# Performance work log

Hardware: AMD Instinct MI355X
Metric: run time of the kernel (lower is better)

Reference implementation:

```python
import jax, jax.numpy as jnp
import numpy as np

B = 32        # number of graphs
NPG = 2048    # nodes per graph (equal sizes -> max_size == NPG)
N = B * NPG   # total nodes
DEG = 16      # average degree
E = N * DEG   # total edges
F_IN = 128    # num_node_feats
LATENT = [32, 32, 32, 1]
TOTAL = sum(LATENT)  # 97
K = 30        # phi output size (DGCNN k)
OUT = 32      # output_dim


def setup_inputs() -> dict:
    key = jax.random.key(0)
    ks = jax.random.split(key, 16)
    node_feat = jax.random.normal(ks[0], (N, F_IN), jnp.float32)

    # edges constrained within each graph (block-diagonal n2n adjacency)
    rng = np.random.default_rng(0)
    offsets = np.repeat(np.arange(B, dtype=np.int64) * NPG, NPG * DEG)
    src = rng.integers(0, NPG, size=E) + offsets
    dst = rng.integers(0, NPG, size=E) + offsets
    edge_index = jnp.asarray(np.stack([src, dst]).astype(np.int32))

    # node_degs = in-degree + 1, shape [N, 1]
    degs = np.bincount(dst, minlength=N).astype(np.float32)
    node_degs = jnp.asarray(degs + 1.0)[:, None]

    def lin(k, fan_in, fan_out):
        s = 1.0 / np.sqrt(fan_in)
        kw, kb = jax.random.split(k)
        W = jax.random.uniform(kw, (fan_in, fan_out), jnp.float32, -s, s)
        b = jax.random.uniform(kb, (fan_out,), jnp.float32, -s, s)
        return W, b

    dims = [F_IN] + LATENT
    params = {}
    for i in range(len(LATENT)):
        W, b = lin(ks[1 + i], dims[i], dims[i + 1])
        params[f"W{i}"] = W
        params[f"b{i}"] = b
    params["phi_W"], params["phi_b"] = lin(ks[10], TOTAL, K)
    params["rho_W"], params["rho_b"] = lin(ks[11], K, OUT)

    return dict(node_feat=node_feat, node_degs=node_degs, edge_index=edge_index, **params)


def reference(node_feat, node_degs, W0, b0, W1, b1, W2, b2, W3, b3,
              phi_W, phi_b, rho_W, rho_b, edge_index):
    src, dst = edge_index[0], edge_index[1]
    n = node_feat.shape[0]

    def spmm(x):  # n2n adjacency @ x via gather + segment-sum
        return jax.ops.segment_sum(x[src], dst, num_segments=n)

    h = node_feat
    layers = [(W0, b0), (W1, b1), (W2, b2), (W3, b3)]
    cats = []
    for W, b in layers:
        pooled = spmm(h) + h                       # A h + h
        h = jnp.tanh((pooled @ W + b) / node_degs)  # linear, degree norm, tanh
        cats.append(h)
    msg = jnp.concatenate(cats, axis=1)            # [N, 97]

    # sortpooling-to-batched tensor: equal graph sizes -> pure reshape
    batched = msg.reshape(B, NPG, TOTAL)

    # DeepSets invariant model: rho(sum_i phi(x_i))
    phi = jax.nn.relu(batched @ phi_W + phi_b)     # [B, NPG, K]
    summed = jnp.sum(phi, axis=1)                  # [B, K]
    out = summed @ rho_W + rho_b                   # [B, OUT]
    return out
```

## Files before the change

### kernel.cpp

```cpp
#include <hip/hip_runtime.h>
#include <hip/hip_bf16.h>

#define NN 65536
#define NE (NN * 16)
#define NG 32
#define MAXD 64

#define WS_CURSOR 0
#define WS_SUMMED 262144
#define WS_ELL    1048576
#define WS_ZA     (WS_ELL + NN * MAXD * 4)
#define WS_ZB     (WS_ZA + NN * 32 * 2)
#define WS_H1     (WS_ZB + NN * 32 * 2)
#define WS_H2     (WS_H1 + NN * 32 * 2)
#define WS_H3     (WS_H2 + NN * 32 * 2)
#define WS_Z4     (WS_H3 + NN * 32 * 2)

typedef unsigned short bf16;

__device__ __forceinline__ int xcd_swz(int b, int chunk) {
    return (b & 7) * chunk + (b >> 3);
}

__device__ __forceinline__ float ftanh(float x) {
    float xc = fmaxf(fminf(x, 15.f), -15.f);
    float e = __expf(2.f * xc);
    return (e - 1.f) * __builtin_amdgcn_rcpf(e + 1.f);
}

__device__ __forceinline__ float bf2f(bf16 u) {
    return __uint_as_float(((unsigned int)u) << 16);
}
__device__ __forceinline__ bf16 f2bf(float x) {
    unsigned int b = __float_as_uint(x);
    b += 0x7FFF + ((b >> 16) & 1);
    return (bf16)(b >> 16);
}

__global__ __launch_bounds__(256) void k_build(const int* __restrict__ ei,
                                               int* __restrict__ cursor,
                                               int* __restrict__ ell) {
    int blk = xcd_swz(blockIdx.x, 128);
    int idx = blk * 256 + threadIdx.x;
    const int4* e4 = (const int4*)ei;
    int4 s = e4[idx];
    int4 d = e4[NE / 4 + idx];
    int t;
    t = atomicAdd(&cursor[d.x], 1); if (t < MAXD) ell[d.x * MAXD + t] = s.x;
    t = atomicAdd(&cursor[d.y], 1); if (t < MAXD) ell[d.y * MAXD + t] = s.y;
    t = atomicAdd(&cursor[d.z], 1); if (t < MAXD) ell[d.z * MAXD + t] = s.z;
    t = atomicAdd(&cursor[d.w], 1); if (t < MAXD) ell[d.w * MAXD + t] = s.w;
}

__global__ __launch_bounds__(256) void k_gemm1(const float* __restrict__ feat,
                                               const float* __restrict__ W0,
                                               bf16* __restrict__ z1) {
    __shared__ float wl[32 * 132];
    __shared__ float hl[64 * 132];
    int tid = threadIdx.x;
    for (int i = tid; i < 128 * 32; i += 256) {
        int k = i >> 5, c = i & 31;
        wl[c * 132 + k] = W0[i];
    }
    int base = blockIdx.x * 64;
    const float* fsrc = feat + (size_t)base * 128;
    #pragma unroll
    for (int v = 0; v < 8; ++v) {
        int flat = v * 1024 + tid * 4;
        int rr = flat >> 7, kk = flat & 127;
        *(float4*)&hl[rr * 132 + kk] = *(const float4*)&fsrc[flat];
    }
    __syncthreads();
    int cg = tid & 15, rg = tid >> 4;
    int c0 = cg * 2, r0 = rg * 4;
    float acc[4][2] = {};
    #pragma unroll 2
    for (int k = 0; k < 128; k += 4) {
        float4 wa = *(const float4*)&wl[c0 * 132 + k];
        float4 wb = *(const float4*)&wl[(c0 + 1) * 132 + k];
        #pragma unroll
        for (int rr = 0; rr < 4; ++rr) {
            float4 hv = *(const float4*)&hl[(r0 + rr) * 132 + k];
            acc[rr][0] += hv.x * wa.x + hv.y * wa.y + hv.z * wa.z + hv.w * wa.w;
            acc[rr][1] += hv.x * wb.x + hv.y * wb.y + hv.z * wb.z + hv.w * wb.w;
        }
    }
    #pragma unroll
    for (int rr = 0; rr < 4; ++rr) {
        int d = base + r0 + rr;
        unsigned int pk = (unsigned int)f2bf(acc[rr][0]) |
                          ((unsigned int)f2bf(acc[rr][1]) << 16);
        *(unsigned int*)&z1[(size_t)d * 32 + c0] = pk;
    }
}

#define GB8(iv) do {                                                           \
    int s0=__shfl((iv),0,8), s1=__shfl((iv),1,8), s2=__shfl((iv),2,8), s3=__shfl((iv),3,8); \
    int s4=__shfl((iv),4,8), s5=__shfl((iv),5,8), s6=__shfl((iv),6,8), s7=__shfl((iv),7,8); \
    ushort4 v0=*(const ushort4*)&zin[(size_t)s0*32+q4];                        \
    ushort4 v1=*(const ushort4*)&zin[(size_t)s1*32+q4];                        \
    ushort4 v2=*(const ushort4*)&zin[(size_t)s2*32+q4];                        \
    ushort4 v3=*(const ushort4*)&zin[(size_t)s3*32+q4];                        \
    ushort4 v4=*(const ushort4*)&zin[(size_t)s4*32+q4];                        \
    ushort4 v5=*(const ushort4*)&zin[(size_t)s5*32+q4];                        \
    ushort4 v6=*(const ushort4*)&zin[(size_t)s6*32+q4];                        \
    ushort4 v7=*(const ushort4*)&zin[(size_t)s7*32+q4];                        \
    acc.x += ((bf2f(v0.x)+bf2f(v1.x))+(bf2f(v2.x)+bf2f(v3.x)))                 \
           + ((bf2f(v4.x)+bf2f(v5.x))+(bf2f(v6.x)+bf2f(v7.x)));                \
    acc.y += ((bf2f(v0.y)+bf2f(v1.y))+(bf2f(v2.y)+bf2f(v3.y)))                 \
           + ((bf2f(v4.y)+bf2f(v5.y))+(bf2f(v6.y)+bf2f(v7.y)));                \
    acc.z += ((bf2f(v0.z)+bf2f(v1.z))+(bf2f(v2.z)+bf2f(v3.z)))                 \
           + ((bf2f(v4.z)+bf2f(v5.z))+(bf2f(v6.z)+bf2f(v7.z)));                \
    acc.w += ((bf2f(v0.w)+bf2f(v1.w))+(bf2f(v2.w)+bf2f(v3.w)))                 \
           + ((bf2f(v4.w)+bf2f(v5.w))+(bf2f(v6.w)+bf2f(v7.w)));                \
} while (0)

__device__ __forceinline__ float4 gatherbf(const int* __restrict__ row, int cnt,
                                           const bf16* __restrict__ zin,
                                           int q4, float4 acc) {
    int q = q4 >> 2;
    int i0 = row[q], i1 = row[8 + q], i2 = row[16 + q], i3 = row[24 + q];
    int m = cnt < 32 ? cnt : 32;
    if (m >= 8)  GB8(i0);
    if (m >= 16) GB8(i1);
    if (m >= 24) GB8(i2);
    if (m >= 32) GB8(i3);
    int done = m & ~7;
    if (done < m) {
        int ivr = (done == 0) ? i0 : (done == 8) ? i1 : (done == 16) ? i2 : i3;
        for (int j = done; j < m; ++j) {
            int s = __shfl(ivr, j - done, 8);
            ushort4 v = *(const ushort4*)&zin[(size_t)s * 32 + q4];
            acc.x += bf2f(v.x); acc.y += bf2f(v.y);
            acc.z += bf2f(v.z); acc.w += bf2f(v.w);
        }
    }
    for (int j = 32; j < cnt && j < MAXD; ++j) {
        int s = row[j];
        ushort4 v = *(const ushort4*)&zin[(size_t)s * 32 + q4];
        acc.x += bf2f(v.x); acc.y += bf2f(v.y);
        acc.z += bf2f(v.z); acc.w += bf2f(v.w);
    }
    return acc;
}

__global__ __launch_bounds__(256) void k_layer(const float* __restrict__ degs,
                                               const int* __restrict__ ell,
                                               const bf16* __restrict__ zin,
                                               const float* __restrict__ bias,
                                               const float* __restrict__ Wn,
                                               bf16* __restrict__ hout,
                                               bf16* __restrict__ znext) {
    __shared__ float wt[32 * 36];
    __shared__ float hl[32 * 36];
    int tid = threadIdx.x;
    for (int i = tid; i < 1024; i += 256) {
        int k = i >> 5, c = i & 31;
        wt[c * 36 + k] = Wn[i];
    }
    int blk = xcd_swz(blockIdx.x, 256);
    int r = tid >> 3, q4 = (tid & 7) * 4;
    int d = blk * 32 + r;
    float degv = degs[d];
    int cnt = (int)degv - 1;
    const int* row = ell + (size_t)d * MAXD;
    ushort4 sv = *(const ushort4*)&zin[(size_t)d * 32 + q4];
    float4 acc = {bf2f(sv.x), bf2f(sv.y), bf2f(sv.z), bf2f(sv.w)};
    acc = gatherbf(row, cnt, zin, q4, acc);
    float4 b4 = *(const float4*)&bias[q4];
    float rdeg = __builtin_amdgcn_rcpf(degv);
    float4 val;
    val.x = ftanh((acc.x + b4.x) * rdeg);
    val.y = ftanh((acc.y + b4.y) * rdeg);
    val.z = ftanh((acc.z + b4.z) * rdeg);
    val.w = ftanh((acc.w + b4.w) * rdeg);
    ushort4 hv4 = {f2bf(val.x), f2bf(val.y), f2bf(val.z), f2bf(val.w)};
    *(ushort4*)&hout[(size_t)d * 32 + q4] = hv4;
    *(float4*)&hl[r * 36 + q4] = val;
    __syncthreads();
    #pragma unroll
    for (int it = 0; it < 4; ++it) {
        int wid = tid + it * 256;
        int n = wid >> 5, c = wid & 31;
        const float* hrow = &hl[n * 36];
        const float* wrow = &wt[c * 36];
        float4 a4 = {0.f, 0.f, 0.f, 0.f};
        #pragma unroll
        for (int k = 0; k < 32; k += 4) {
            float4 hv = *(const float4*)&hrow[k];
            float4 wv = *(const float4*)&wrow[k];
            a4.x += hv.x * wv.x; a4.y += hv.y * wv.y;
            a4.z += hv.z * wv.z; a4.w += hv.w * wv.w;
        }
        znext[(size_t)(blk * 32 + n) * 32 + c] =
            f2bf((a4.x + a4.y) + (a4.z + a4.w));
    }
}

__global__ __launch_bounds__(256) void k_layer3(const float* __restrict__ degs,
                                                const int* __restrict__ ell,
                                                const bf16* __restrict__ zin,
                                                const float* __restrict__ bias,
                                                const float* __restrict__ W3,
                                                bf16* __restrict__ hout,
                                                float* __restrict__ z4) {
    int tid = threadIdx.x;
    int blk = xcd_swz(blockIdx.x, 256);
    int r = tid >> 3, q4 = (tid & 7) * 4;
    int d = blk * 32 + r;
    float degv = degs[d];
    int cnt = (int)degv - 1;
    const int* row = ell + (size_t)d * MAXD;
    ushort4 sv = *(const ushort4*)&zin[(size_t)d * 32 + q4];
    float4 acc = {bf2f(sv.x), bf2f(sv.y), bf2f(sv.z), bf2f(sv.w)};
    acc = gatherbf(row, cnt, zin, q4, acc);
    float4 b4 = *(const float4*)&bias[q4];
    float rdeg = __builtin_amdgcn_rcpf(degv);
    float4 val;
    val.x = ftanh((acc.x + b4.x) * rdeg);
    val.y = ftanh((acc.y + b4.y) * rdeg);
    val.z = ftanh((acc.z + b4.z) * rdeg);
    val.w = ftanh((acc.w + b4.w) * rdeg);
    ushort4 hv4 = {f2bf(val.x), f2bf(val.y), f2bf(val.z), f2bf(val.w)};
    *(ushort4*)&hout[(size_t)d * 32 + q4] = hv4;
    float4 w4 = *(const float4*)&W3[q4];
    float v = (val.x * w4.x + val.y * w4.y) + (val.z * w4.z + val.w * w4.w);
    v += __shfl_xor(v, 1, 8);
    v += __shfl_xor(v, 2, 8);
    v += __shfl_xor(v, 4, 8);
    if ((tid & 7) == 0) z4[d] = v;
}

__global__ __launch_bounds__(512) void k_phi(const float* __restrict__ degs,
                                             const int* __restrict__ ell,
                                             const float* __restrict__ z4,
                                             const float* __restrict__ b3,
                                             const bf16* __restrict__ h1,
                                             const bf16* __restrict__ h2,
                                             const bf16* __restrict__ h3,
                                             const float* __restrict__ phiW,
                                             const float* __restrict__ phib,
                                             float* __restrict__ summed) {
    __shared__ float pl[30 * 100];
    __shared__ float ml[16 * 100];
    __shared__ float part[8][32];
    int tid = threadIdx.x;
    for (int i = tid; i < 30 * 97; i += 512) {
        int cc = i / 97, jj = i - cc * 97;
        pl[cc * 100 + jj] = phiW[jj * 30 + cc];
    }
    int blk = xcd_swz(blockIdx.x, 512);
    int r = tid >> 5, c = tid & 31;
    int d = blk * 16 + r;
    int g = d >> 11;
    float degv = degs[d];
    int cnt = (int)degv - 1; if (cnt > MAXD) cnt = MAXD;
    const int* row = ell + (size_t)d * MAXD;
    float acc = 0.f;
    for (int j = c; j < cnt; j += 32) acc += z4[row[j]];
    #pragma unroll
    for (int off = 16; off; off >>= 1) acc += __shfl_xor(acc, off, 32);
    float h4 = ftanh((acc + z4[d] + b3[0]) * __builtin_amdgcn_rcpf(degv));
    ml[r * 100 + c]      = bf2f(h1[(size_t)d * 32 + c]);
    ml[r * 100 + 32 + c] = bf2f(h2[(size_t)d * 32 + c]);
    ml[r * 100 + 64 + c] = bf2f(h3[(size_t)d * 32 + c]);
    if (c == 0) ml[r * 100 + 96] = h4;
    __syncthreads();
    float s = 0.f;
    if (c < 30) {
        const float* mrow = ml + r * 100;
        const float* prow = pl + c * 100;
        float4 a4 = {0.f, 0.f, 0.f, 0.f};
        #pragma unroll
        for (int j = 0; j < 96; j += 4) {
            float4 mv = *(const float4*)&mrow[j];
            float4 pv = *(const float4*)&prow[j];
            a4.x += mv.x * pv.x; a4.y += mv.y * pv.y;
            a4.z += mv.z * pv.z; a4.w += mv.w * pv.w;
        }
        s = (a4.x + a4.y) + (a4.z + a4.w) + mrow[96] * prow[96] + phib[c];
        s = fmaxf(s, 0.f);
    }
    s += __shfl_down(s, 32);
    int wave = tid >> 6;
    if ((tid & 63) < 32) part[wave][tid & 31] = s;
    __syncthreads();
    if (tid < 32) {
        float tot = 0.f;
        #pragma unroll
        for (int w = 0; w < 8; ++w) tot += part[w][tid];
        if (tid < 30) atomicAdd(&summed[g * 30 + tid], tot);
    }
}

__global__ __launch_bounds__(1024) void k_rho(const float* __restrict__ summed,
                                              const float* __restrict__ rhoW,
                                              const float* __restrict__ rhob,
                                              float* __restrict__ out) {
    int tid = threadIdx.x;
    int b = tid >> 5, o = tid & 31;
    float s = rhob[o];
    #pragma unroll
    for (int k = 0; k < 30; ++k) s += summed[b * 30 + k] * rhoW[k * 32 + o];
    out[tid] = s;
}

extern "C" void kernel_launch(void* const* d_in, const int* in_sizes, int n_in,
                              void* d_out, int out_size, void* d_ws, size_t ws_size,
                              hipStream_t stream) {
    const float* feat = (const float*)d_in[0];
    const float* degs = (const float*)d_in[1];
    const int*   ei   = (const int*)d_in[2];
    const float* W0   = (const float*)d_in[3];
    const float* b0   = (const float*)d_in[4];
    const float* W1   = (const float*)d_in[5];
    const float* b1   = (const float*)d_in[6];
    const float* W2   = (const float*)d_in[7];
    const float* b2   = (const float*)d_in[8];
    const float* W3   = (const float*)d_in[9];
    const float* b3   = (const float*)d_in[10];
    const float* phiW = (const float*)d_in[11];
    const float* phib = (const float*)d_in[12];
    const float* rhoW = (const float*)d_in[13];
    const float* rhob = (const float*)d_in[14];

    char* ws = (char*)d_ws;
    int*   cursor = (int*)(ws + WS_CURSOR);
    float* summed = (float*)(ws + WS_SUMMED);
    int*   ell    = (int*)(ws + WS_ELL);
    bf16*  za     = (bf16*)(ws + WS_ZA);
    bf16*  zb     = (bf16*)(ws + WS_ZB);
    bf16*  h1     = (bf16*)(ws + WS_H1);
    bf16*  h2     = (bf16*)(ws + WS_H2);
    bf16*  h3     = (bf16*)(ws + WS_H3);
    float* z4     = (float*)(ws + WS_Z4);
    float* out    = (float*)d_out;

    hipMemsetAsync(ws, 0, WS_SUMMED + NG * 30 * 4, stream);

    k_build <<<NE / 1024, 256, 0, stream>>>(ei, cursor, ell);
    k_gemm1 <<<NN / 64, 256, 0, stream>>>(feat, W0, za);
    k_layer <<<NN / 32, 256, 0, stream>>>(degs, ell, za, b0, W1, h1, zb);
    k_layer <<<NN / 32, 256, 0, stream>>>(degs, ell, zb, b1, W2, h2, za);
    k_layer3<<<NN / 32, 256, 0, stream>>>(degs, ell, za, b2, W3, h3, z4);
    k_phi   <<<NN / 16, 512, 0, stream>>>(degs, ell, z4, b3, h1, h2, h3, phiW, phib, summed);
    k_rho   <<<1, 1024, 0, stream>>>(summed, rhoW, rhob, out);
}
```

Baseline: 259.9 us.

## Stage per-graph feature tables in LDS for neighbor gathers

```diff
diff --git a/kernel.cpp b/kernel.cpp
--- a/kernel.cpp
+++ b/kernel.cpp
@@ -94,17 +94,19 @@
     }
 }
 
-#define GB8(iv) do {                                                           \
-    int s0=__shfl((iv),0,8), s1=__shfl((iv),1,8), s2=__shfl((iv),2,8), s3=__shfl((iv),3,8); \
-    int s4=__shfl((iv),4,8), s5=__shfl((iv),5,8), s6=__shfl((iv),6,8), s7=__shfl((iv),7,8); \
-    ushort4 v0=*(const ushort4*)&zin[(size_t)s0*32+q4];                        \
-    ushort4 v1=*(const ushort4*)&zin[(size_t)s1*32+q4];                        \
-    ushort4 v2=*(const ushort4*)&zin[(size_t)s2*32+q4];                        \
-    ushort4 v3=*(const ushort4*)&zin[(size_t)s3*32+q4];                        \
-    ushort4 v4=*(const ushort4*)&zin[(size_t)s4*32+q4];                        \
-    ushort4 v5=*(const ushort4*)&zin[(size_t)s5*32+q4];                        \
-    ushort4 v6=*(const ushort4*)&zin[(size_t)s6*32+q4];                        \
-    ushort4 v7=*(const ushort4*)&zin[(size_t)s7*32+q4];                        \
+#define GB8L(iv) do {                                                          \
+    int s0=__shfl((iv),0,8)&2047, s1=__shfl((iv),1,8)&2047;                    \
+    int s2=__shfl((iv),2,8)&2047, s3=__shfl((iv),3,8)&2047;                    \
+    int s4=__shfl((iv),4,8)&2047, s5=__shfl((iv),5,8)&2047;                    \
+    int s6=__shfl((iv),6,8)&2047, s7=__shfl((iv),7,8)&2047;                    \
+    ushort4 v0=*(const ushort4*)&zl[s0*32+q4];                                 \
+    ushort4 v1=*(const ushort4*)&zl[s1*32+q4];                                 \
+    ushort4 v2=*(const ushort4*)&zl[s2*32+q4];                                 \
+    ushort4 v3=*(const ushort4*)&zl[s3*32+q4];                                 \
+    ushort4 v4=*(const ushort4*)&zl[s4*32+q4];                                 \
+    ushort4 v5=*(const ushort4*)&zl[s5*32+q4];                                 \
+    ushort4 v6=*(const ushort4*)&zl[s6*32+q4];                                 \
+    ushort4 v7=*(const ushort4*)&zl[s7*32+q4];                                 \
     acc.x += ((bf2f(v0.x)+bf2f(v1.x))+(bf2f(v2.x)+bf2f(v3.x)))                 \
            + ((bf2f(v4.x)+bf2f(v5.x))+(bf2f(v6.x)+bf2f(v7.x)));                \
     acc.y += ((bf2f(v0.y)+bf2f(v1.y))+(bf2f(v2.y)+bf2f(v3.y)))                 \
@@ -115,120 +117,169 @@
            + ((bf2f(v4.w)+bf2f(v5.w))+(bf2f(v6.w)+bf2f(v7.w)));                \
 } while (0)
 
-__device__ __forceinline__ float4 gatherbf(const int* __restrict__ row, int cnt,
-                                           const bf16* __restrict__ zin,
-                                           int q4, float4 acc) {
+__device__ __forceinline__ float4 gatherlds(const int* __restrict__ row, int cnt,
+                                            const bf16* zl, int q4, float4 acc) {
     int q = q4 >> 2;
     int i0 = row[q], i1 = row[8 + q], i2 = row[16 + q], i3 = row[24 + q];
     int m = cnt < 32 ? cnt : 32;
-    if (m >= 8)  GB8(i0);
-    if (m >= 16) GB8(i1);
-    if (m >= 24) GB8(i2);
-    if (m >= 32) GB8(i3);
+    if (m >= 8)  GB8L(i0);
+    if (m >= 16) GB8L(i1);
+    if (m >= 24) GB8L(i2);
+    if (m >= 32) GB8L(i3);
     int done = m & ~7;
     if (done < m) {
         int ivr = (done == 0) ? i0 : (done == 8) ? i1 : (done == 16) ? i2 : i3;
         for (int j = done; j < m; ++j) {
-            int s = __shfl(ivr, j - done, 8);
-            ushort4 v = *(const ushort4*)&zin[(size_t)s * 32 + q4];
+            int s = __shfl(ivr, j - done, 8) & 2047;
+            ushort4 v = *(const ushort4*)&zl[s * 32 + q4];
             acc.x += bf2f(v.x); acc.y += bf2f(v.y);
             acc.z += bf2f(v.z); acc.w += bf2f(v.w);
         }
     }
     for (int j = 32; j < cnt && j < MAXD; ++j) {
-        int s = row[j];
-        ushort4 v = *(const ushort4*)&zin[(size_t)s * 32 + q4];
+        int s = row[j] & 2047;
+        ushort4 v = *(const ushort4*)&zl[s * 32 + q4];
         acc.x += bf2f(v.x); acc.y += bf2f(v.y);
         acc.z += bf2f(v.z); acc.w += bf2f(v.w);
     }
     return acc;
 }
 
-__global__ __launch_bounds__(256) void k_layer(const float* __restrict__ degs,
-                                               const int* __restrict__ ell,
-                                               const bf16* __restrict__ zin,
-                                               const float* __restrict__ bias,
-                                               const float* __restrict__ Wn,
-                                               bf16* __restrict__ hout,
-                                               bf16* __restrict__ znext) {
-    __shared__ float wt[32 * 36];
-    __shared__ float hl[32 * 36];
+__global__ __launch_bounds__(1024) void k_layer(const float* __restrict__ degs,
+                                                const int* __restrict__ ell,
+                                                const bf16* __restrict__ zin,
+                                                const float* __restrict__ bias,
+                                                const float* __restrict__ Wn,
+                                                bf16* __restrict__ hout,
+                                                bf16* __restrict__ znext) {
+    __shared__ __align__(16) unsigned char smem[131072];
+    bf16*  zl = (bf16*)smem;
+    float* hl = (float*)smem;
+    float* wt = (float*)(smem + 256 * 36 * 4);
     int tid = threadIdx.x;
-    for (int i = tid; i < 1024; i += 256) {
-        int k = i >> 5, c = i & 31;
-        wt[c * 36 + k] = Wn[i];
-    }
-    int blk = xcd_swz(blockIdx.x, 256);
-    int r = tid >> 3, q4 = (tid & 7) * 4;
-    int d = blk * 32 + r;
-    float degv = degs[d];
-    int cnt = (int)degv - 1;
-    const int* row = ell + (size_t)d * MAXD;
-    ushort4 sv = *(const ushort4*)&zin[(size_t)d * 32 + q4];
-    float4 acc = {bf2f(sv.x), bf2f(sv.y), bf2f(sv.z), bf2f(sv.w)};
-    acc = gatherbf(row, cnt, zin, q4, acc);
-    float4 b4 = *(const float4*)&bias[q4];
-    float rdeg = __builtin_amdgcn_rcpf(degv);
-    float4 val;
-    val.x = ftanh((acc.x + b4.x) * rdeg);
-    val.y = ftanh((acc.y + b4.y) * rdeg);
-    val.z = ftanh((acc.z + b4.z) * rdeg);
-    val.w = ftanh((acc.w + b4.w) * rdeg);
-    ushort4 hv4 = {f2bf(val.x), f2bf(val.y), f2bf(val.z), f2bf(val.w)};
-    *(ushort4*)&hout[(size_t)d * 32 + q4] = hv4;
-    *(float4*)&hl[r * 36 + q4] = val;
-    __syncthreads();
-    #pragma unroll
-    for (int it = 0; it < 4; ++it) {
-        int wid = tid + it * 256;
-        int n = wid >> 5, c = wid & 31;
-        const float* hrow = &hl[n * 36];
-        const float* wrow = &wt[c * 36];
-        float4 a4 = {0.f, 0.f, 0.f, 0.f};
+    int blk = xcd_swz(blockIdx.x, 32);
+    int g = blk >> 3;
+    int nbase = (blk & 7) << 8;
+    const bf16* zg = zin + (((size_t)g << 11) << 5);
+    {
+        const uint4* src = (const uint4*)zg;
+        uint4* dst = (uint4*)smem;
+        #pragma unroll
+        for (int i = 0; i < 8; ++i) dst[tid + i * 1024] = src[tid + i * 1024];
+    }
+    __syncthreads();
+
+    int grp = tid >> 3, q4 = (tid & 7) * 4;
+    float4 val[2];
+    #pragma unroll
+    for (int it = 0; it < 2; ++it) {
+        int rr = grp + it * 128;
+        int dl = nbase + rr;
+        int d  = (g << 11) + dl;
+        float degv = degs[d];
+        int cnt = (int)degv - 1;
+        const int* row = ell + (size_t)d * MAXD;
+        ushort4 sv = *(const ushort4*)&zl[dl * 32 + q4];
+        float4 acc = {bf2f(sv.x), bf2f(sv.y), bf2f(sv.z), bf2f(sv.w)};
+        acc = gatherlds(row, cnt, zl, q4, acc);
+        float4 b4 = *(const float4*)&bias[q4];
+        float rdeg = __builtin_amdgcn_rcpf(degv);
+        val[it].x = ftanh((acc.x + b4.x) * rdeg);
+        val[it].y = ftanh((acc.y + b4.y) * rdeg);
+        val[it].z = ftanh((acc.z + b4.z) * rdeg);
+        val[it].w = ftanh((acc.w + b4.w) * rdeg);
+        ushort4 hv4 = {f2bf(val[it].x), f2bf(val[it].y),
+                       f2bf(val[it].z), f2bf(val[it].w)};
+        *(ushort4*)&hout[(size_t)d * 32 + q4] = hv4;
+    }
+    __syncthreads();
+
+    #pragma unroll
+    for (int it = 0; it < 2; ++it) {
+        int rr = grp + it * 128;
+        *(float4*)&hl[rr * 36 + q4] = val[it];
+    }
+    if (tid < 1024) {
+        int k = tid >> 5, c = tid & 31;
+        wt[c * 36 + k] = Wn[tid];
+    }
+    __syncthreads();
+
+    int n = tid >> 2, c0 = (tid & 3) * 8;
+    const float* hrow = &hl[n * 36];
+    float o[8];
+    #pragma unroll
+    for (int cc = 0; cc < 8; ++cc) {
+        const float* wrow = &wt[(c0 + cc) * 36];
+        float4 a = {0.f, 0.f, 0.f, 0.f};
         #pragma unroll
         for (int k = 0; k < 32; k += 4) {
             float4 hv = *(const float4*)&hrow[k];
             float4 wv = *(const float4*)&wrow[k];
-            a4.x += hv.x * wv.x; a4.y += hv.y * wv.y;
-            a4.z += hv.z * wv.z; a4.w += hv.w * wv.w;
+            a.x += hv.x * wv.x; a.y += hv.y * wv.y;
+            a.z += hv.z * wv.z; a.w += hv.w * wv.w;
         }
-        znext[(size_t)(blk * 32 + n) * 32 + c] =
-            f2bf((a4.x + a4.y) + (a4.z + a4.w));
-    }
-}
-
-__global__ __launch_bounds__(256) void k_layer3(const float* __restrict__ degs,
-                                                const int* __restrict__ ell,
-                                                const bf16* __restrict__ zin,
-                                                const float* __restrict__ bias,
-                                                const float* __restrict__ W3,
-                                                bf16* __restrict__ hout,
-                                                float* __restrict__ z4) {
+        o[cc] = (a.x + a.y) + (a.z + a.w);
+    }
+    int dn = (g << 11) + nbase + n;
+    uint4 pk;
+    pk.x = (unsigned int)f2bf(o[0]) | ((unsigned int)f2bf(o[1]) << 16);
+    pk.y = (unsigned int)f2bf(o[2]) | ((unsigned int)f2bf(o[3]) << 16);
+    pk.z = (unsigned int)f2bf(o[4]) | ((unsigned int)f2bf(o[5]) << 16);
+    pk.w = (unsigned int)f2bf(o[6]) | ((unsigned int)f2bf(o[7]) << 16);
+    *(uint4*)&znext[(size_t)dn * 32 + c0] = pk;
+}
+
+__global__ __launch_bounds__(1024) void k_layer3(const float* __restrict__ degs,
+                                                 const int* __restrict__ ell,
+                                                 const bf16* __restrict__ zin,
+                                                 const float* __restrict__ bias,
+                                                 const float* __restrict__ W3,
+                                                 bf16* __restrict__ hout,
+                                                 float* __restrict__ z4) {
+    __shared__ __align__(16) unsigned char smem[131072];
+    bf16* zl = (bf16*)smem;
     int tid = threadIdx.x;
-    int blk = xcd_swz(blockIdx.x, 256);
-    int r = tid >> 3, q4 = (tid & 7) * 4;
-    int d = blk * 32 + r;
-    float degv = degs[d];
-    int cnt = (int)degv - 1;
-    const int* row = ell + (size_t)d * MAXD;
-    ushort4 sv = *(const ushort4*)&zin[(size_t)d * 32 + q4];
-    float4 acc = {bf2f(sv.x), bf2f(sv.y), bf2f(sv.z), bf2f(sv.w)};
-    acc = gatherbf(row, cnt, zin, q4, acc);
-    float4 b4 = *(const float4*)&bias[q4];
-    float rdeg = __builtin_amdgcn_rcpf(degv);
-    float4 val;
-    val.x = ftanh((acc.x + b4.x) * rdeg);
-    val.y = ftanh((acc.y + b4.y) * rdeg);
-    val.z = ftanh((acc.z + b4.z) * rdeg);
-    val.w = ftanh((acc.w + b4.w) * rdeg);
-    ushort4 hv4 = {f2bf(val.x), f2bf(val.y), f2bf(val.z), f2bf(val.w)};
-    *(ushort4*)&hout[(size_t)d * 32 + q4] = hv4;
+    int blk = xcd_swz(blockIdx.x, 32);
+    int g = blk >> 3;
+    int nbase = (blk & 7) << 8;
+    const bf16* zg = zin + (((size_t)g << 11) << 5);
+    {
+        const uint4* src = (const uint4*)zg;
+        uint4* dst = (uint4*)smem;
+        #pragma unroll
+        for (int i = 0; i < 8; ++i) dst[tid + i * 1024] = src[tid + i * 1024];
+    }
+    __syncthreads();
+
+    int grp = tid >> 3, q = tid & 7, q4 = q * 4;
     float4 w4 = *(const float4*)&W3[q4];
-    float v = (val.x * w4.x + val.y * w4.y) + (val.z * w4.z + val.w * w4.w);
-    v += __shfl_xor(v, 1, 8);
-    v += __shfl_xor(v, 2, 8);
-    v += __shfl_xor(v, 4, 8);
-    if ((tid & 7) == 0) z4[d] = v;
+    #pragma unroll
+    for (int it = 0; it < 2; ++it) {
+        int rr = grp + it * 128;
+        int dl = nbase + rr;
+        int d  = (g << 11) + dl;
+        float degv = degs[d];
+        int cnt = (int)degv - 1;
+        const int* row = ell + (size_t)d * MAXD;
+        ushort4 sv = *(const ushort4*)&zl[dl * 32 + q4];
+        float4 acc = {bf2f(sv.x), bf2f(sv.y), bf2f(sv.z), bf2f(sv.w)};
+        acc = gatherlds(row, cnt, zl, q4, acc);
+        float4 b4 = *(const float4*)&bias[q4];
+        float rdeg = __builtin_amdgcn_rcpf(degv);
+        float4 val;
+        val.x = ftanh((acc.x + b4.x) * rdeg);
+        val.y = ftanh((acc.y + b4.y) * rdeg);
+        val.z = ftanh((acc.z + b4.z) * rdeg);
+        val.w = ftanh((acc.w + b4.w) * rdeg);
+        ushort4 hv4 = {f2bf(val.x), f2bf(val.y), f2bf(val.z), f2bf(val.w)};
+        *(ushort4*)&hout[(size_t)d * 32 + q4] = hv4;
+        float v = (val.x * w4.x + val.y * w4.y) + (val.z * w4.z + val.w * w4.w);
+        v += __shfl_xor(v, 1, 8);
+        v += __shfl_xor(v, 2, 8);
+        v += __shfl_xor(v, 4, 8);
+        if (q == 0) z4[d] = v;
+    }
 }
 
 __global__ __launch_bounds__(512) void k_phi(const float* __restrict__ degs,
@@ -244,6 +295,7 @@
     __shared__ float pl[30 * 100];
     __shared__ float ml[16 * 100];
     __shared__ float part[8][32];
+    __shared__ float z4l[2048];
     int tid = threadIdx.x;
     for (int i = tid; i < 30 * 97; i += 512) {
         int cc = i / 97, jj = i - cc * 97;
@@ -253,14 +305,17 @@
     int r = tid >> 5, c = tid & 31;
     int d = blk * 16 + r;
     int g = d >> 11;
+    const float* z4g = z4 + ((size_t)g << 11);
+    for (int i = tid; i < 2048; i += 512) z4l[i] = z4g[i];
+    __syncthreads();
     float degv = degs[d];
     int cnt = (int)degv - 1; if (cnt > MAXD) cnt = MAXD;
     const int* row = ell + (size_t)d * MAXD;
     float acc = 0.f;
-    for (int j = c; j < cnt; j += 32) acc += z4[row[j]];
+    for (int j = c; j < cnt; j += 32) acc += z4l[row[j] & 2047];
     #pragma unroll
     for (int off = 16; off; off >>= 1) acc += __shfl_xor(acc, off, 32);
-    float h4 = ftanh((acc + z4[d] + b3[0]) * __builtin_amdgcn_rcpf(degv));
+    float h4 = ftanh((acc + z4l[d & 2047] + b3[0]) * __builtin_amdgcn_rcpf(degv));
     ml[r * 100 + c]      = bf2f(h1[(size_t)d * 32 + c]);
     ml[r * 100 + 32 + c] = bf2f(h2[(size_t)d * 32 + c]);
     ml[r * 100 + 64 + c] = bf2f(h3[(size_t)d * 32 + c]);
@@ -340,9 +395,9 @@
 
     k_build <<<NE / 1024, 256, 0, stream>>>(ei, cursor, ell);
     k_gemm1 <<<NN / 64, 256, 0, stream>>>(feat, W0, za);
-    k_layer <<<NN / 32, 256, 0, stream>>>(degs, ell, za, b0, W1, h1, zb);
-    k_layer <<<NN / 32, 256, 0, stream>>>(degs, ell, zb, b1, W2, h2, za);
-    k_layer3<<<NN / 32, 256, 0, stream>>>(degs, ell, za, b2, W3, h3, z4);
+    k_layer <<<NN / 256, 1024, 0, stream>>>(degs, ell, za, b0, W1, h1, zb);
+    k_layer <<<NN / 256, 1024, 0, stream>>>(degs, ell, zb, b1, W2, h2, za);
+    k_layer3<<<NN / 256, 1024, 0, stream>>>(degs, ell, za, b2, W3, h3, z4);
     k_phi   <<<NN / 16, 512, 0, stream>>>(degs, ell, z4, b3, h1, h2, h3, phiW, phib, summed);
     k_rho   <<<1, 1024, 0, stream>>>(summed, rhoW, rhob, out);
 }
```

Measured after the change: 311.8 us. +20.0%, slower.

## Build ELL adjacency per graph slice with LDS atomics instead of global atomics

Applied to the files above, without the earlier changes.

```diff
diff --git a/kernel.cpp b/kernel.cpp
--- a/kernel.cpp
+++ b/kernel.cpp
@@ -37,19 +37,31 @@
     return (bf16)(b >> 16);
 }
 
-__global__ __launch_bounds__(256) void k_build(const int* __restrict__ ei,
-                                               int* __restrict__ cursor,
-                                               int* __restrict__ ell) {
-    int blk = xcd_swz(blockIdx.x, 128);
-    int idx = blk * 256 + threadIdx.x;
-    const int4* e4 = (const int4*)ei;
-    int4 s = e4[idx];
-    int4 d = e4[NE / 4 + idx];
-    int t;
-    t = atomicAdd(&cursor[d.x], 1); if (t < MAXD) ell[d.x * MAXD + t] = s.x;
-    t = atomicAdd(&cursor[d.y], 1); if (t < MAXD) ell[d.y * MAXD + t] = s.y;
-    t = atomicAdd(&cursor[d.z], 1); if (t < MAXD) ell[d.z * MAXD + t] = s.z;
-    t = atomicAdd(&cursor[d.w], 1); if (t < MAXD) ell[d.w * MAXD + t] = s.w;
+#define BB_SUB 16
+#define BB_RANGE (2048 / BB_SUB)
+
+__global__ __launch_bounds__(1024) void k_build(const int* __restrict__ ei,
+                                                int* __restrict__ ell) {
+    __shared__ int lcnt[BB_RANGE];
+    int tid = threadIdx.x;
+    int blk = xcd_swz(blockIdx.x, 64);
+    int g = blk >> 4, sub = blk & 15;
+    int dbase = (g << 11) + sub * BB_RANGE;
+    if (tid < BB_RANGE) lcnt[tid] = 0;
+    __syncthreads();
+    const int4* s4 = (const int4*)ei + ((size_t)g << 13);
+    const int4* d4 = (const int4*)(ei + NE) + ((size_t)g << 13);
+    #pragma unroll
+    for (int it = 0; it < 8; ++it) {
+        int i = it * 1024 + tid;
+        int4 s = s4[i];
+        int4 d = d4[i];
+        int r, t;
+        r = d.x - dbase; if ((unsigned)r < BB_RANGE) { t = atomicAdd(&lcnt[r], 1); if (t < MAXD) ell[d.x * MAXD + t] = s.x; }
+        r = d.y - dbase; if ((unsigned)r < BB_RANGE) { t = atomicAdd(&lcnt[r], 1); if (t < MAXD) ell[d.y * MAXD + t] = s.y; }
+        r = d.z - dbase; if ((unsigned)r < BB_RANGE) { t = atomicAdd(&lcnt[r], 1); if (t < MAXD) ell[d.z * MAXD + t] = s.z; }
+        r = d.w - dbase; if ((unsigned)r < BB_RANGE) { t = atomicAdd(&lcnt[r], 1); if (t < MAXD) ell[d.w * MAXD + t] = s.w; }
+    }
 }
 
 __global__ __launch_bounds__(256) void k_gemm1(const float* __restrict__ feat,
@@ -325,7 +337,6 @@
     const float* rhob = (const float*)d_in[14];
 
     char* ws = (char*)d_ws;
-    int*   cursor = (int*)(ws + WS_CURSOR);
     float* summed = (float*)(ws + WS_SUMMED);
     int*   ell    = (int*)(ws + WS_ELL);
     bf16*  za     = (bf16*)(ws + WS_ZA);
@@ -336,9 +347,9 @@
     float* z4     = (float*)(ws + WS_Z4);
     float* out    = (float*)d_out;
 
-    hipMemsetAsync(ws, 0, WS_SUMMED + NG * 30 * 4, stream);
-
-    k_build <<<NE / 1024, 256, 0, stream>>>(ei, cursor, ell);
+    hipMemsetAsync(ws + WS_SUMMED, 0, NG * 30 * 4, stream);
+
+    k_build <<<512, 1024, 0, stream>>>(ei, ell);
     k_gemm1 <<<NN / 64, 256, 0, stream>>>(feat, W0, za);
     k_layer <<<NN / 32, 256, 0, stream>>>(degs, ell, za, b0, W1, h1, zb);
     k_layer <<<NN / 32, 256, 0, stream>>>(degs, ell, zb, b1, W2, h2, za);
```

Result: faster. 215.4 us (-17.1%).
